# Kernel optimization log

Measured on AMD Instinct MI355X. Metric: run time of the kernel, lower is better.

Reference implementation:

```python
import jax, jax.numpy as jnp
import numpy as np

B, N, D = 32768, 50, 128  # batch, neighbours, embedding_dim


def setup_inputs() -> dict:
    key = jax.random.key(0)
    k1, k2, k3, k4 = jax.random.split(key, 4)
    scale = 1.0 / np.sqrt(D)
    return {
        "mainNodeEmbed": jax.random.normal(k1, (B, D), dtype=jnp.float32),
        "neighbourNodesEmbeds": jax.random.normal(k2, (B, N, D), dtype=jnp.float32),
        "W": jax.random.normal(k3, (D, D), dtype=jnp.float32) * scale,            # self.w kernel (no bias)
        "A_w": jax.random.normal(k4, (2 * D, D), dtype=jnp.float32) * scale,      # attentionDense kernel
        "A_b": jnp.zeros((D,), dtype=jnp.float32),                                 # attentionDense bias
    }


def reference(mainNodeEmbed, neighbourNodesEmbeds, W, A_w, A_b):
    # Linear projections (shared weight, no bias)
    px = mainNodeEmbed @ W                       # [B, D]
    pn = neighbourNodesEmbeds @ W                # [B, N, D]
    # mode == 'repeat': tile main node across neighbours, concat on feature dim
    px_rep = jnp.broadcast_to(px[:, None, :], pn.shape)   # [B, N, D]
    cat = jnp.concatenate([px_rep, pn], axis=2)           # [B, N, 2D]
    # attention logits: Dense + leaky_relu (tf default alpha=0.2)
    e_ij = jax.nn.leaky_relu(cat @ A_w + A_b, negative_slope=0.2)  # [B, N, D]
    # softmax over the neighbour axis (axis=1), per feature channel
    a_ij = jax.nn.softmax(e_ij, axis=1)
    # attention-weighted sum over neighbours
    return jnp.sum(a_ij * pn, axis=1)            # [B, D]
```

## Files before the change

### kernel.cpp

```cpp
#include <hip/hip_runtime.h>
#include <math.h>

#define NN 50
#define DD 128
#define MT 4
#define KT 4
#define NIT 32
#define TILE_B 25600
#define NPASS 25

typedef __attribute__((ext_vector_type(4))) float  f32x4;
typedef __attribute__((ext_vector_type(2))) __fp16 f16x2;
typedef __attribute__((ext_vector_type(8))) __fp16 f16x8;

__device__ float g_WA1f[DD * DD];
__device__ float g_WA2f[DD * DD];
__device__ __attribute__((aligned(16))) __fp16 g_Wt[2 * DD * DD];
__device__ __attribute__((aligned(16))) __fp16 g_W1t[DD * DD];

__global__ void compute_WA(const float* __restrict__ W,
                           const float* __restrict__ A_w) {
    const int d = threadIdx.x, k = blockIdx.x, m = blockIdx.y;
    const float* __restrict__ A = A_w + (size_t)m * DD * DD;
    float acc = 0.f;
#pragma unroll 8
    for (int j = 0; j < DD; ++j)
        acc = fmaf(W[k * DD + j], A[j * DD + d], acc);
    if (m == 0) g_WA1f[k * DD + d] = acc;
    else        g_WA2f[k * DD + d] = acc;
}

__global__ void cvt_weights(const float* __restrict__ W) {
    const int n = blockIdx.x;
    const int k = threadIdx.x;
    if (n < DD)          g_Wt[n * DD + k]             = (__fp16)W[k * DD + n];
    else if (n < 2 * DD) g_Wt[n * DD + k]             = (__fp16)g_WA2f[k * DD + (n - DD)];
    else                 g_W1t[(n - 2 * DD) * DD + k] = (__fp16)g_WA1f[k * DD + (n - 2 * DD)];
}

__device__ __forceinline__ f16x8 cvt8(float4 f0, float4 f1) {
    union { f16x2 h[4]; f16x8 v; } u;
    u.h[0] = __builtin_amdgcn_cvt_pkrtz(f0.x, f0.y);
    u.h[1] = __builtin_amdgcn_cvt_pkrtz(f0.z, f0.w);
    u.h[2] = __builtin_amdgcn_cvt_pkrtz(f1.x, f1.y);
    u.h[3] = __builtin_amdgcn_cvt_pkrtz(f1.z, f1.w);
    return u.v;
}

#define MFMA(a, b, c) __builtin_amdgcn_mfma_f32_16x16x32_f16((a), (b), (c), 0, 0, 0)

__global__ __launch_bounds__(256, 2)
void attn_mfma(const float* __restrict__ x,
               const float* __restrict__ nbr,
               const float* __restrict__ A_b,
               float* __restrict__ out, int B) {
    __shared__ __attribute__((aligned(16))) char tiles[2][TILE_B];
    __shared__ float pxa_lds[NIT][DD + 4];

    const int tid  = threadIdx.x;
    const int w    = tid >> 6;
    const int lane = tid & 63;
    const int c    = lane & 15;
    const int g    = lane >> 4;
    const int bb   = blockIdx.x;
    const int grid = gridDim.x;

    {
        f32x4 pacc[NIT / 16][2];
#pragma unroll
        for (int mt = 0; mt < NIT / 16; ++mt)
#pragma unroll
            for (int nt = 0; nt < 2; ++nt) pacc[mt][nt] = (f32x4)0.f;

#pragma unroll
        for (int mt = 0; mt < NIT / 16; ++mt) {
            long brow = (long)bb + (long)grid * (16 * mt + c);
            if (brow > B - 1) brow = B - 1;
            const float4* __restrict__ xp =
                reinterpret_cast<const float4*>(x + brow * DD);
#pragma unroll
            for (int kt = 0; kt < KT; ++kt) {
                const f16x8 a = cvt8(xp[8 * kt + 2 * g], xp[8 * kt + 2 * g + 1]);
#pragma unroll
                for (int nt = 0; nt < 2; ++nt) {
                    const int col = 32 * w + 16 * nt + c;
                    const f16x8 bw = *reinterpret_cast<const f16x8*>(
                        g_W1t + col * DD + 32 * kt + 8 * g);
                    pacc[mt][nt] = MFMA(a, bw, pacc[mt][nt]);
                }
            }
        }
        const float ab0 = A_b[32 * w + c];
        const float ab1 = A_b[32 * w + 16 + c];
#pragma unroll
        for (int mt = 0; mt < NIT / 16; ++mt)
#pragma unroll
            for (int nt = 0; nt < 2; ++nt)
#pragma unroll
                for (int r = 0; r < 4; ++r)
                    pxa_lds[16 * mt + 4 * g + r][32 * w + 16 * nt + c] =
                        pacc[mt][nt][r] + (nt ? ab1 : ab0);
    }

    f16x8 bF[2][2][KT];
#pragma unroll
    for (int p = 0; p < 2; ++p)
#pragma unroll
        for (int nt = 0; nt < 2; ++nt)
#pragma unroll
            for (int kt = 0; kt < KT; ++kt) {
                const int col = p * DD + 32 * w + 16 * nt + c;
                bF[p][nt][kt] = *reinterpret_cast<const f16x8*>(
                    g_Wt + col * DD + 32 * kt + 8 * g);
                asm volatile("" : "+v"(bF[p][nt][kt]));
            }

    __syncthreads();

    auto stage = [&](int it, int bufidx) {
        const char* nb = (const char*)(nbr + (size_t)(bb + (size_t)grid * it) * (NN * DD));
#pragma unroll
        for (int j = 0; j < 7; ++j) {
            const int p = w + 4 * j;
            if (p < NPASS) {
                const int dloc = p * 1024 + lane * 16;
                const int row  = dloc >> 9;
                const int src  = dloc ^ ((row & 7) << 4);
                __builtin_amdgcn_global_load_lds(
                    (const __attribute__((address_space(1))) void*)(nb + src),
                    (__attribute__((address_space(3))) void*)(&tiles[bufidx][p * 1024]),
                    16, 0, 0);
            }
        }
    };

    stage(0, 0);
    stage(1, 1);

    const float m0v = (g == 0) ? 1.f : 0.f;

#pragma unroll 1
    for (int i = 0; i < NIT; ++i) {
        asm volatile("s_waitcnt vmcnt(6)" ::: "memory");
        __builtin_amdgcn_s_barrier();

        const char* __restrict__ tile = tiles[i & 1];
        f32x4 acc[MT][2][2];
#pragma unroll
        for (int mt = 0; mt < MT; ++mt)
#pragma unroll
            for (int p = 0; p < 2; ++p)
#pragma unroll
                for (int nt = 0; nt < 2; ++nt) acc[mt][p][nt] = (f32x4)0.f;

#pragma unroll
        for (int mt = 0; mt < MT; ++mt) {
            int row = 16 * mt + c;
            if (row > NN - 1) row = NN - 1;
            const int rb = row * 512;
            const int sw = (row & 7) << 4;
            f16x8 afr[KT];
#pragma unroll
            for (int kt = 0; kt < KT; ++kt) {
                const int off = rb + kt * 128 + g * 32;
                const float4 lo = *(const float4*)(tile + ((off) ^ sw));
                const float4 hi = *(const float4*)(tile + ((off + 16) ^ sw));
                afr[kt] = cvt8(lo, hi);
            }
#pragma unroll
            for (int kt = 0; kt < KT; ++kt)
#pragma unroll
                for (int p = 0; p < 2; ++p)
#pragma unroll
                    for (int nt = 0; nt < 2; ++nt)
                        acc[mt][p][nt] = MFMA(afr[kt], bF[p][nt][kt], acc[mt][p][nt]);
        }

#pragma unroll
        for (int nt = 0; nt < 2; ++nt) {
            const int col = 32 * w + 16 * nt + c;
            const float pxa = pxa_lds[i][col];
            float den = 0.f, num = 0.f;
#pragma unroll
            for (int mt = 0; mt < MT; ++mt)
#pragma unroll
                for (int r = 0; r < 4; ++r) {
                    if (mt == 3 && r >= 2) continue;
                    float t = pxa + acc[mt][1][nt][r];
                    t = fmaxf(t, 0.2f * t);
                    float p = __expf(t);
                    if (mt == 3) p *= m0v;
                    den += p;
                    num = fmaf(p, acc[mt][0][nt][r], num);
                }
            den += __shfl_xor(den, 16); den += __shfl_xor(den, 32);
            num += __shfl_xor(num, 16); num += __shfl_xor(num, 32);
            if (g == 0) out[(size_t)(bb + (size_t)grid * i) * DD + col] =
                __fdividef(num, den);
        }

        asm volatile("s_waitcnt lgkmcnt(0)" ::: "memory");
        __builtin_amdgcn_sched_barrier(0);
        __builtin_amdgcn_s_barrier();

        int t2 = i + 2;
        if (t2 > NIT - 1) t2 = NIT - 1;
        stage(t2, i & 1);
    }
}

extern "C" void kernel_launch(void* const* d_in, const int* in_sizes, int n_in,
                              void* d_out, int out_size, void* d_ws, size_t ws_size,
                              hipStream_t stream) {
    const float* x   = (const float*)d_in[0];
    const float* nbr = (const float*)d_in[1];
    const float* W   = (const float*)d_in[2];
    const float* A_w = (const float*)d_in[3];
    const float* A_b = (const float*)d_in[4];
    float* out = (float*)d_out;
    const int B = in_sizes[0] / DD;

    compute_WA<<<dim3(DD, 2), DD, 0, stream>>>(W, A_w);
    cvt_weights<<<3 * DD, DD, 0, stream>>>(W);
    const int grid = (B + NIT - 1) / NIT;
    attn_mfma<<<grid, 256, 0, stream>>>(x, nbr, A_b, out, B);
}
```

Measured before the change: 254.9 us.

## Split column work across 8 waves per block and drop redundant tail loads

The block grows from 4 to 8 waves, and each wave now owns 16 output columns instead of 32. This halves per-wave accumulators and B-fragment registers and spreads the neighbour-tile staging over more waves. The final two iterations no longer reload the last tile; they issue dummy 4-byte loads into a scratch LDS buffer so the vmcnt accounting stays fixed. The padding on pxa_lds is removed. The intent is more latency hiding through more resident waves and lower register pressure, at the cost of extra barrier participants and every wave recomputing the same A-fragment conversions.

```diff
diff --git a/kernel.cpp b/kernel.cpp
--- a/kernel.cpp
+++ b/kernel.cpp
@@ -49,13 +49,14 @@
 
 #define MFMA(a, b, c) __builtin_amdgcn_mfma_f32_16x16x32_f16((a), (b), (c), 0, 0, 0)
 
-__global__ __launch_bounds__(256, 2)
+__global__ __launch_bounds__(512, 4)
 void attn_mfma(const float* __restrict__ x,
                const float* __restrict__ nbr,
                const float* __restrict__ A_b,
                float* __restrict__ out, int B) {
     __shared__ __attribute__((aligned(16))) char tiles[2][TILE_B];
-    __shared__ float pxa_lds[NIT][DD + 4];
+    __shared__ float pxa_lds[NIT][DD];
+    __shared__ __attribute__((aligned(16))) char dummy_lds[256];
 
     const int tid  = threadIdx.x;
     const int w    = tid >> 6;
@@ -66,11 +67,9 @@
     const int grid = gridDim.x;
 
     {
-        f32x4 pacc[NIT / 16][2];
-#pragma unroll
-        for (int mt = 0; mt < NIT / 16; ++mt)
-#pragma unroll
-            for (int nt = 0; nt < 2; ++nt) pacc[mt][nt] = (f32x4)0.f;
+        f32x4 pacc[NIT / 16];
+#pragma unroll
+        for (int mt = 0; mt < NIT / 16; ++mt) pacc[mt] = (f32x4)0.f;
 
 #pragma unroll
         for (int mt = 0; mt < NIT / 16; ++mt) {
@@ -81,48 +80,39 @@
 #pragma unroll
             for (int kt = 0; kt < KT; ++kt) {
                 const f16x8 a = cvt8(xp[8 * kt + 2 * g], xp[8 * kt + 2 * g + 1]);
-#pragma unroll
-                for (int nt = 0; nt < 2; ++nt) {
-                    const int col = 32 * w + 16 * nt + c;
-                    const f16x8 bw = *reinterpret_cast<const f16x8*>(
-                        g_W1t + col * DD + 32 * kt + 8 * g);
-                    pacc[mt][nt] = MFMA(a, bw, pacc[mt][nt]);
-                }
+                const f16x8 bw = *reinterpret_cast<const f16x8*>(
+                    g_W1t + (16 * w + c) * DD + 32 * kt + 8 * g);
+                pacc[mt] = MFMA(a, bw, pacc[mt]);
             }
         }
-        const float ab0 = A_b[32 * w + c];
-        const float ab1 = A_b[32 * w + 16 + c];
+        const float ab = A_b[16 * w + c];
 #pragma unroll
         for (int mt = 0; mt < NIT / 16; ++mt)
 #pragma unroll
-            for (int nt = 0; nt < 2; ++nt)
-#pragma unroll
-                for (int r = 0; r < 4; ++r)
-                    pxa_lds[16 * mt + 4 * g + r][32 * w + 16 * nt + c] =
-                        pacc[mt][nt][r] + (nt ? ab1 : ab0);
+            for (int r = 0; r < 4; ++r)
+                pxa_lds[16 * mt + 4 * g + r][16 * w + c] = pacc[mt][r] + ab;
     }
 
-    f16x8 bF[2][2][KT];
+    f16x8 bF[2][KT];
 #pragma unroll
     for (int p = 0; p < 2; ++p)
 #pragma unroll
-        for (int nt = 0; nt < 2; ++nt)
-#pragma unroll
-            for (int kt = 0; kt < KT; ++kt) {
-                const int col = p * DD + 32 * w + 16 * nt + c;
-                bF[p][nt][kt] = *reinterpret_cast<const f16x8*>(
-                    g_Wt + col * DD + 32 * kt + 8 * g);
-                asm volatile("" : "+v"(bF[p][nt][kt]));
-            }
+        for (int kt = 0; kt < KT; ++kt) {
+            const int col = p * DD + 16 * w + c;
+            bF[p][kt] = *reinterpret_cast<const f16x8*>(
+                g_Wt + col * DD + 32 * kt + 8 * g);
+            asm volatile("" : "+v"(bF[p][kt]));
+        }
 
     __syncthreads();
 
     auto stage = [&](int it, int bufidx) {
-        const char* nb = (const char*)(nbr + (size_t)(bb + (size_t)grid * it) * (NN * DD));
-#pragma unroll
-        for (int j = 0; j < 7; ++j) {
-            const int p = w + 4 * j;
-            if (p < NPASS) {
+        const char* nb = (const char*)(nbr +
+            (size_t)(bb + (size_t)grid * (it < 0 ? 0 : it)) * (NN * DD));
+#pragma unroll
+        for (int j = 0; j < 4; ++j) {
+            const int p = w + 8 * j;
+            if (it >= 0 && p < NPASS) {
                 const int dloc = p * 1024 + lane * 16;
                 const int row  = dloc >> 9;
                 const int src  = dloc ^ ((row & 7) << 4);
@@ -130,6 +120,10 @@
                     (const __attribute__((address_space(1))) void*)(nb + src),
                     (__attribute__((address_space(3))) void*)(&tiles[bufidx][p * 1024]),
                     16, 0, 0);
+            } else {
+                __builtin_amdgcn_global_load_lds(
+                    (const __attribute__((address_space(1))) void*)x,
+                    (__attribute__((address_space(3))) void*)dummy_lds, 4, 0, 0);
             }
         }
     };
@@ -141,17 +135,15 @@
 
 #pragma unroll 1
     for (int i = 0; i < NIT; ++i) {
-        asm volatile("s_waitcnt vmcnt(6)" ::: "memory");
+        asm volatile("s_waitcnt vmcnt(4)" ::: "memory");
         __builtin_amdgcn_s_barrier();
 
         const char* __restrict__ tile = tiles[i & 1];
-        f32x4 acc[MT][2][2];
+        f32x4 acc[MT][2];
 #pragma unroll
         for (int mt = 0; mt < MT; ++mt)
 #pragma unroll
-            for (int p = 0; p < 2; ++p)
-#pragma unroll
-                for (int nt = 0; nt < 2; ++nt) acc[mt][p][nt] = (f32x4)0.f;
+            for (int p = 0; p < 2; ++p) acc[mt][p] = (f32x4)0.f;
 
 #pragma unroll
         for (int mt = 0; mt < MT; ++mt) {
@@ -171,31 +163,27 @@
             for (int kt = 0; kt < KT; ++kt)
 #pragma unroll
                 for (int p = 0; p < 2; ++p)
-#pragma unroll
-                    for (int nt = 0; nt < 2; ++nt)
-                        acc[mt][p][nt] = MFMA(afr[kt], bF[p][nt][kt], acc[mt][p][nt]);
-        }
-
-#pragma unroll
-        for (int nt = 0; nt < 2; ++nt) {
-            const int col = 32 * w + 16 * nt + c;
-            const float pxa = pxa_lds[i][col];
+                    acc[mt][p] = MFMA(afr[kt], bF[p][kt], acc[mt][p]);
+        }
+
+        {
+            const float pxa = pxa_lds[i][16 * w + c];
             float den = 0.f, num = 0.f;
 #pragma unroll
             for (int mt = 0; mt < MT; ++mt)
 #pragma unroll
                 for (int r = 0; r < 4; ++r) {
                     if (mt == 3 && r >= 2) continue;
-                    float t = pxa + acc[mt][1][nt][r];
+                    float t = pxa + acc[mt][1][r];
                     t = fmaxf(t, 0.2f * t);
                     float p = __expf(t);
                     if (mt == 3) p *= m0v;
                     den += p;
-                    num = fmaf(p, acc[mt][0][nt][r], num);
+                    num = fmaf(p, acc[mt][0][r], num);
                 }
             den += __shfl_xor(den, 16); den += __shfl_xor(den, 32);
             num += __shfl_xor(num, 16); num += __shfl_xor(num, 32);
-            if (g == 0) out[(size_t)(bb + (size_t)grid * i) * DD + col] =
+            if (g == 0) out[(size_t)(bb + (size_t)grid * i) * DD + 16 * w + c] =
                 __fdividef(num, den);
         }
 
@@ -203,9 +191,8 @@
         __builtin_amdgcn_sched_barrier(0);
         __builtin_amdgcn_s_barrier();
 
-        int t2 = i + 2;
-        if (t2 > NIT - 1) t2 = NIT - 1;
-        stage(t2, i & 1);
+        const int t2 = i + 2;
+        stage(t2 < NIT ? t2 : -1, i & 1);
     }
 }
 
@@ -223,5 +210,5 @@
     compute_WA<<<dim3(DD, 2), DD, 0, stream>>>(W, A_w);
     cvt_weights<<<3 * DD, DD, 0, stream>>>(W);
     const int grid = (B + NIT - 1) / NIT;
-    attn_mfma<<<grid, 256, 0, stream>>>(x, nbr, A_b, out, B);
-}
+    attn_mfma<<<grid, 512, 0, stream>>>(x, nbr, A_b, out, B);
+}
```

New measurement: 271.6 us. 6.6% more time.

## Fold main-node projection into neighbour tile and triple-buffer contiguous batch blocks

Applied to the files above, without the earlier changes.

Drops the per-block prologue GEMM that computed the main-node attention term into LDS. Instead the main-node row is loaded as a 51st row of each neighbour tile, and its projection comes from extra MFMAs in the last M-tile, broadcast with a shuffle. Also moves to three LDS buffers with the next stage issued before the wait, contiguous batch blocks of 64 items, and dummy loads to keep vmcnt accounting uniform. This adds LDS per block and extra MFMA work in exchange for removing the prologue and getting deeper prefetch.

```diff
diff --git a/kernel.cpp b/kernel.cpp
--- a/kernel.cpp
+++ b/kernel.cpp
@@ -5,9 +5,10 @@
 #define DD 128
 #define MT 4
 #define KT 4
-#define NIT 32
-#define TILE_B 25600
-#define NPASS 25
+#define NIT 64
+#define ROWS 51
+#define TILE_B (ROWS * 512)
+#define NBUF 3
 
 typedef __attribute__((ext_vector_type(4))) float  f32x4;
 typedef __attribute__((ext_vector_type(2))) __fp16 f16x2;
@@ -15,8 +16,7 @@
 
 __device__ float g_WA1f[DD * DD];
 __device__ float g_WA2f[DD * DD];
-__device__ __attribute__((aligned(16))) __fp16 g_Wt[2 * DD * DD];
-__device__ __attribute__((aligned(16))) __fp16 g_W1t[DD * DD];
+__device__ __attribute__((aligned(16))) __fp16 g_Wt[3 * DD * DD];
 
 __global__ void compute_WA(const float* __restrict__ W,
                            const float* __restrict__ A_w) {
@@ -33,9 +33,11 @@
 __global__ void cvt_weights(const float* __restrict__ W) {
     const int n = blockIdx.x;
     const int k = threadIdx.x;
-    if (n < DD)          g_Wt[n * DD + k]             = (__fp16)W[k * DD + n];
-    else if (n < 2 * DD) g_Wt[n * DD + k]             = (__fp16)g_WA2f[k * DD + (n - DD)];
-    else                 g_W1t[(n - 2 * DD) * DD + k] = (__fp16)g_WA1f[k * DD + (n - 2 * DD)];
+    float v;
+    if (n < DD)          v = W[k * DD + n];
+    else if (n < 2 * DD) v = g_WA2f[k * DD + (n - DD)];
+    else                 v = g_WA1f[k * DD + (n - 2 * DD)];
+    g_Wt[n * DD + k] = (__fp16)v;
 }
 
 __device__ __forceinline__ f16x8 cvt8(float4 f0, float4 f1) {
@@ -54,57 +56,19 @@
                const float* __restrict__ nbr,
                const float* __restrict__ A_b,
                float* __restrict__ out, int B) {
-    __shared__ __attribute__((aligned(16))) char tiles[2][TILE_B];
-    __shared__ float pxa_lds[NIT][DD + 4];
+    __shared__ __attribute__((aligned(16))) char tiles[NBUF][TILE_B];
+    __shared__ __attribute__((aligned(16))) char dummy_lds[64];
 
     const int tid  = threadIdx.x;
     const int w    = tid >> 6;
     const int lane = tid & 63;
     const int c    = lane & 15;
     const int g    = lane >> 4;
-    const int bb   = blockIdx.x;
-    const int grid = gridDim.x;
-
-    {
-        f32x4 pacc[NIT / 16][2];
-#pragma unroll
-        for (int mt = 0; mt < NIT / 16; ++mt)
-#pragma unroll
-            for (int nt = 0; nt < 2; ++nt) pacc[mt][nt] = (f32x4)0.f;
-
-#pragma unroll
-        for (int mt = 0; mt < NIT / 16; ++mt) {
-            long brow = (long)bb + (long)grid * (16 * mt + c);
-            if (brow > B - 1) brow = B - 1;
-            const float4* __restrict__ xp =
-                reinterpret_cast<const float4*>(x + brow * DD);
-#pragma unroll
-            for (int kt = 0; kt < KT; ++kt) {
-                const f16x8 a = cvt8(xp[8 * kt + 2 * g], xp[8 * kt + 2 * g + 1]);
-#pragma unroll
-                for (int nt = 0; nt < 2; ++nt) {
-                    const int col = 32 * w + 16 * nt + c;
-                    const f16x8 bw = *reinterpret_cast<const f16x8*>(
-                        g_W1t + col * DD + 32 * kt + 8 * g);
-                    pacc[mt][nt] = MFMA(a, bw, pacc[mt][nt]);
-                }
-            }
-        }
-        const float ab0 = A_b[32 * w + c];
-        const float ab1 = A_b[32 * w + 16 + c];
-#pragma unroll
-        for (int mt = 0; mt < NIT / 16; ++mt)
-#pragma unroll
-            for (int nt = 0; nt < 2; ++nt)
-#pragma unroll
-                for (int r = 0; r < 4; ++r)
-                    pxa_lds[16 * mt + 4 * g + r][32 * w + 16 * nt + c] =
-                        pacc[mt][nt][r] + (nt ? ab1 : ab0);
-    }
-
-    f16x8 bF[2][2][KT];
-#pragma unroll
-    for (int p = 0; p < 2; ++p)
+    const size_t b0 = (size_t)blockIdx.x * NIT;
+
+    f16x8 bF[3][2][KT];
+#pragma unroll
+    for (int p = 0; p < 3; ++p)
 #pragma unroll
         for (int nt = 0; nt < 2; ++nt)
 #pragma unroll
@@ -114,49 +78,78 @@
                     g_Wt + col * DD + 32 * kt + 8 * g);
                 asm volatile("" : "+v"(bF[p][nt][kt]));
             }
-
-    __syncthreads();
-
-    auto stage = [&](int it, int bufidx) {
-        const char* nb = (const char*)(nbr + (size_t)(bb + (size_t)grid * it) * (NN * DD));
+    float ab0 = A_b[32 * w + c];
+    float ab1 = A_b[32 * w + 16 + c];
+    asm volatile("" : "+v"(ab0), "+v"(ab1));
+
+    auto stage = [&](int it, char* dst) {
+        const size_t bidx = b0 + (size_t)(it < 0 ? 0 : it);
+        const char* nb = (const char*)(nbr + bidx * (NN * DD));
+        const char* xb = (const char*)(x + bidx * DD);
 #pragma unroll
         for (int j = 0; j < 7; ++j) {
             const int p = w + 4 * j;
-            if (p < NPASS) {
+            if (it >= 0 && p < 25) {
                 const int dloc = p * 1024 + lane * 16;
                 const int row  = dloc >> 9;
                 const int src  = dloc ^ ((row & 7) << 4);
                 __builtin_amdgcn_global_load_lds(
                     (const __attribute__((address_space(1))) void*)(nb + src),
-                    (__attribute__((address_space(3))) void*)(&tiles[bufidx][p * 1024]),
+                    (__attribute__((address_space(3))) void*)(dst + p * 1024),
                     16, 0, 0);
+            } else if (it >= 0 && p == 25) {
+                if (lane < 32) {
+                    const int src = (lane * 16) ^ ((50 & 7) << 4);
+                    __builtin_amdgcn_global_load_lds(
+                        (const __attribute__((address_space(1))) void*)(xb + src),
+                        (__attribute__((address_space(3))) void*)(dst + 50 * 512),
+                        16, 0, 0);
+                }
+            } else {
+                __builtin_amdgcn_global_load_lds(
+                    (const __attribute__((address_space(1))) void*)x,
+                    (__attribute__((address_space(3))) void*)dummy_lds, 4, 0, 0);
             }
         }
     };
 
-    stage(0, 0);
-    stage(1, 1);
+    char* bufA = tiles[0];
+    char* bufB = tiles[1];
+    char* bufC = tiles[2];
+
+    stage(0, bufA);
+    stage(1, bufB);
+#pragma unroll
+    for (int j = 0; j < 4; ++j)
+        __builtin_amdgcn_global_load_lds(
+            (const __attribute__((address_space(1))) void*)x,
+            (__attribute__((address_space(3))) void*)dummy_lds, 4, 0, 0);
 
     const float m0v = (g == 0) ? 1.f : 0.f;
 
 #pragma unroll 1
     for (int i = 0; i < NIT; ++i) {
-        asm volatile("s_waitcnt vmcnt(6)" ::: "memory");
+        const int t2 = i + 2;
+        stage(t2 < NIT ? t2 : -1, bufC);
+
+        asm volatile("s_waitcnt vmcnt(18)" ::: "memory");
         __builtin_amdgcn_s_barrier();
 
-        const char* __restrict__ tile = tiles[i & 1];
+        const char* __restrict__ tile = bufA;
         f32x4 acc[MT][2][2];
+        f32x4 acc2[2];
 #pragma unroll
         for (int mt = 0; mt < MT; ++mt)
 #pragma unroll
             for (int p = 0; p < 2; ++p)
 #pragma unroll
                 for (int nt = 0; nt < 2; ++nt) acc[mt][p][nt] = (f32x4)0.f;
+        acc2[0] = (f32x4)0.f; acc2[1] = (f32x4)0.f;
 
 #pragma unroll
         for (int mt = 0; mt < MT; ++mt) {
             int row = 16 * mt + c;
-            if (row > NN - 1) row = NN - 1;
+            if (row > 50) row = 50;
             const int rb = row * 512;
             const int sw = (row & 7) << 4;
             f16x8 afr[KT];
@@ -174,12 +167,18 @@
 #pragma unroll
                     for (int nt = 0; nt < 2; ++nt)
                         acc[mt][p][nt] = MFMA(afr[kt], bF[p][nt][kt], acc[mt][p][nt]);
+            if (mt == 3) {
+#pragma unroll
+                for (int kt = 0; kt < KT; ++kt)
+#pragma unroll
+                    for (int nt = 0; nt < 2; ++nt)
+                        acc2[nt] = MFMA(afr[kt], bF[2][nt][kt], acc2[nt]);
+            }
         }
 
 #pragma unroll
         for (int nt = 0; nt < 2; ++nt) {
-            const int col = 32 * w + 16 * nt + c;
-            const float pxa = pxa_lds[i][col];
+            const float pxa = __shfl(acc2[nt][2], c) + (nt ? ab1 : ab0);
             float den = 0.f, num = 0.f;
 #pragma unroll
             for (int mt = 0; mt < MT; ++mt)
@@ -195,7 +194,7 @@
                 }
             den += __shfl_xor(den, 16); den += __shfl_xor(den, 32);
             num += __shfl_xor(num, 16); num += __shfl_xor(num, 32);
-            if (g == 0) out[(size_t)(bb + (size_t)grid * i) * DD + col] =
+            if (g == 0) out[(b0 + i) * DD + 32 * w + 16 * nt + c] =
                 __fdividef(num, den);
         }
 
@@ -203,9 +202,7 @@
         __builtin_amdgcn_sched_barrier(0);
         __builtin_amdgcn_s_barrier();
 
-        int t2 = i + 2;
-        if (t2 > NIT - 1) t2 = NIT - 1;
-        stage(t2, i & 1);
+        char* t0 = bufA; bufA = bufB; bufB = bufC; bufC = t0;
     }
 }
 
```

Result: no change. 252.6 us (-0.9%).
